# Kernel tuning notes

Measured on AMD Instinct MI355X. Metric: run time of the kernel, lower is better.

The kernel has to match this reference:

```python
import jax, jax.numpy as jnp
import numpy as np
from jax import lax

EPS = 1e-5

def _conv(x, w, stride, padding):
    # x: NCHW, w: OIHW
    return lax.conv_general_dilated(
        x, w, window_strides=(stride, stride), padding=padding,
        dimension_numbers=("NCHW", "OIHW", "NCHW"))

def _bn(x, gamma, beta):
    # BatchNorm2d in training mode: batch statistics over (N, H, W)
    mean = jnp.mean(x, axis=(0, 2, 3), keepdims=True)
    var = jnp.var(x, axis=(0, 2, 3), keepdims=True)
    inv = lax.rsqrt(var + EPS)
    g = gamma.reshape(1, -1, 1, 1)
    b = beta.reshape(1, -1, 1, 1)
    return (x - mean) * inv * g + b

def setup_inputs() -> dict:
    key = jax.random.key(0)
    ks = jax.random.split(key, 5)
    B, Cin, H, W = 128, 64, 56, 56
    Cout = 128
    x = jax.random.normal(ks[0], (B, Cin, H, W), dtype=jnp.float32)
    w1 = jax.random.normal(ks[1], (Cout, Cin, 3, 3), dtype=jnp.float32) * 0.05
    w2 = jax.random.normal(ks[2], (Cout, Cout, 3, 3), dtype=jnp.float32) * 0.05
    wd = jax.random.normal(ks[3], (Cout, Cin, 1, 1), dtype=jnp.float32) * 0.05
    g1 = jnp.ones((Cout,), jnp.float32); b1 = jnp.zeros((Cout,), jnp.float32)
    g2 = jnp.ones((Cout,), jnp.float32); b2 = jnp.zeros((Cout,), jnp.float32)
    gd = jnp.ones((Cout,), jnp.float32); bd = jnp.zeros((Cout,), jnp.float32)
    return {"x": x, "w1": w1, "g1": g1, "b1": b1,
            "w2": w2, "g2": g2, "b2": b2,
            "wd": wd, "gd": gd, "bd": bd}

def reference(x, w1, g1, b1, w2, g2, b2, wd, gd, bd):
    stride = 2
    # conv1 (3x3, stride=2, 'same') -> BN -> ReLU
    out = _conv(x, w1, stride, "SAME")
    out = jax.nn.relu(_bn(out, g1, b1))
    # conv2 (3x3, stride=1, 'same') -> BN
    out = _conv(out, w2, 1, "SAME")
    out = _bn(out, g2, b2)
    # downsample identity: 1x1 conv stride=2 'valid' -> BN
    identity = _bn(_conv(x, wd, stride, "VALID"), gd, bd)
    return jax.nn.relu(out + identity)
```

## Files before the change

### kernel.cpp

```cpp
#include <hip/hip_runtime.h>

constexpr int B = 128, Cin = 64, H = 56, W = 56;
constexpr int Cout = 128, Ho = 28, Wo = 28;
constexpr int HW = Ho * Wo;
constexpr int NPIX = B * HW;
constexpr int NOUT = NPIX * Cout;
constexpr int NBLK = NPIX / 128;
constexpr int NBLK2 = NPIX / 256;
constexpr float EPS_ = 1e-5f;
constexpr float CNT_ = (float)NPIX;

constexpr int HPX = 57, WPX = 57;
constexpr int HP1 = 30, WP1 = 30;

typedef __attribute__((ext_vector_type(8))) unsigned short u16x8;
typedef __attribute__((ext_vector_type(4))) unsigned short u16x4;
typedef __attribute__((ext_vector_type(8))) short bf16x8;
typedef __attribute__((ext_vector_type(4))) float f32x4;

__device__ inline float bf2f(unsigned short u) {
    union { unsigned int i; float f; } v; v.i = ((unsigned int)u) << 16; return v.f;
}
__device__ inline unsigned short f2bf(float f) {
    union { float f; unsigned int i; } v; v.f = f;
    return (unsigned short)((v.i + 0x7fffu + ((v.i >> 16) & 1u)) >> 16);
}

__device__ inline void gload16(const void* g, void* l) {
    __builtin_amdgcn_global_load_lds(
        (const __attribute__((address_space(1))) unsigned int*)g,
        (__attribute__((address_space(3))) unsigned int*)l, 16, 0, 0);
}

__global__ __launch_bounds__(512) void k_conv2_mfma(
        const unsigned short* __restrict__ xin,
        const unsigned short* __restrict__ wt,
        unsigned short* __restrict__ yout,
        float* __restrict__ part) {
    constexpr int CIN = 128, WP = 30, KTOT = 1152, NSTEP = 36;
    __shared__ unsigned short Alds[3][256 * 32];
    __shared__ unsigned short Blds[3][128 * 32];
    __shared__ float lsum[8][64], lsq[8][64];
    const int tid = threadIdx.x, w = tid >> 6, l = tid & 63;
    const int wr = w >> 1, wc = w & 1;
    const int bid = (blockIdx.x & 7) * (NBLK2 / 8) + (blockIdx.x >> 3);
    const int p0 = bid * 256;
    const char* xb = (const char*)xin;
    const char* wb = (const char*)wt;

    const int sslot = ((l & 3) ^ ((l >> 3) & 3)) * 16;
    const int rswz  = ((l >> 4) ^ ((l >> 1) & 3)) * 16;

    int gA[2], lofsA[2];
    #pragma unroll
    for (int i = 0; i < 2; ++i) {
        int row = w * 32 + i * 16 + (l >> 2);
        int p = p0 + row;
        int n = p / HW, rr = p % HW;
        int oh = rr / Wo, ow = rr % Wo;
        gA[i] = (((n * HP1 + oh) * WP + ow) * CIN) * 2 + sslot;
        lofsA[i] = row * 64 + (l & 3) * 16;
    }
    const int rowb = w * 16 + (l >> 2);
    const int gB = rowb * KTOT * 2 + sslot;
    const int lofsB = rowb * 64 + (l & 3) * 16;

    f32x4 acc[4][4];
    #pragma unroll
    for (int m = 0; m < 4; ++m)
        #pragma unroll
        for (int n = 0; n < 4; ++n)
            acc[m][n] = (f32x4){0.f, 0.f, 0.f, 0.f};

    gload16(xb + gA[0],      (char*)Alds[0] + lofsA[0]);
    gload16(xb + gA[1],      (char*)Alds[0] + lofsA[1]);
    gload16(wb + gB,         (char*)Blds[0] + lofsB);
    gload16(xb + gA[0] + 64, (char*)Alds[1] + lofsA[0]);
    gload16(xb + gA[1] + 64, (char*)Alds[1] + lofsA[1]);
    gload16(wb + gB + 64,    (char*)Blds[1] + lofsB);

    for (int oi = 0; oi < 3; ++oi) {
        const int Abase = oi * WP * CIN * 2;
        #pragma unroll
        for (int u = 0; u < 12; ++u) {
            const int s = oi * 12 + u;
            const int cur = u % 3;
            if (s + 1 < NSTEP) asm volatile("s_waitcnt vmcnt(3)" ::: "memory");
            else               asm volatile("s_waitcnt vmcnt(0)" ::: "memory");
            __builtin_amdgcn_s_barrier();
            if (s + 2 < NSTEP) {
                const int u2 = u + 2;
                const int j2 = u2 >> 2;
                const int c2 = u2 & 3;
                const int koffA = Abase + (j2 == 3 ? WP * CIN * 2 : j2 * CIN * 2) + c2 * 64;
                const int koffB = (s + 2) * 64;
                const int buf = u2 % 3;
                gload16(xb + gA[0] + koffA, (char*)Alds[buf] + lofsA[0]);
                gload16(xb + gA[1] + koffA, (char*)Alds[buf] + lofsA[1]);
                gload16(wb + gB + koffB,    (char*)Blds[buf] + lofsB);
            }
            bf16x8 bf[4];
            #pragma unroll
            for (int n = 0; n < 4; ++n)
                bf[n] = *(const bf16x8*)((const char*)Blds[cur] + (wc * 64 + n * 16 + (l & 15)) * 64 + rswz);
            #pragma unroll
            for (int m = 0; m < 4; ++m) {
                bf16x8 af = *(const bf16x8*)((const char*)Alds[cur] + (wr * 64 + m * 16 + (l & 15)) * 64 + rswz);
                #pragma unroll
                for (int n = 0; n < 4; ++n)
                    acc[m][n] = __builtin_amdgcn_mfma_f32_16x16x32_bf16(af, bf[n], acc[m][n], 0, 0, 0);
            }
        }
    }

    #pragma unroll
    for (int m = 0; m < 4; ++m) {
        int pq = p0 + wr * 64 + m * 16 + (l >> 4) * 4;
        int n = pq / HW, rr = pq % HW;
        #pragma unroll
        for (int q = 0; q < 4; ++q) {
            int co = wc * 64 + q * 16 + (l & 15);
            u16x4 v;
            #pragma unroll
            for (int r = 0; r < 4; ++r) v[r] = f2bf(acc[m][q][r]);
            *(u16x4*)(yout + ((size_t)(n * Cout + co)) * HW + rr) = v;
        }
    }

    float ps[4], pq_[4];
    #pragma unroll
    for (int n = 0; n < 4; ++n) {
        float s_ = 0.f, q_ = 0.f;
        #pragma unroll
        for (int m = 0; m < 4; ++m)
            #pragma unroll
            for (int r = 0; r < 4; ++r) { float v = acc[m][n][r]; s_ += v; q_ += v * v; }
        s_ += __shfl_xor(s_, 16); q_ += __shfl_xor(q_, 16);
        s_ += __shfl_xor(s_, 32); q_ += __shfl_xor(q_, 32);
        ps[n] = s_; pq_[n] = q_;
    }
    __syncthreads();
    if (l < 16) {
        #pragma unroll
        for (int n = 0; n < 4; ++n) { lsum[w][n * 16 + l] = ps[n]; lsq[w][n * 16 + l] = pq_[n]; }
    }
    __syncthreads();
    if (tid < 128) {
        int c = tid, half = c >> 6, j = c & 63;
        float s_ = 0.f, q_ = 0.f;
        #pragma unroll
        for (int r = 0; r < 4; ++r) { s_ += lsum[r * 2 + half][j]; q_ += lsq[r * 2 + half][j]; }
        part[((size_t)bid * 128 + c) * 2]     = s_;
        part[((size_t)bid * 128 + c) * 2 + 1] = q_;
    }
}

template<int STRIDE, int HP, int WP, int CIN, int KHW, bool OUTPAD, bool FUSE_DW>
__global__ __launch_bounds__(256) void k_conv_mfma(
        const unsigned short* __restrict__ xin,
        const unsigned short* __restrict__ wt,
        unsigned short* __restrict__ yout,
        float* __restrict__ part,
        const unsigned short* __restrict__ wtd,
        unsigned short* __restrict__ ydout,
        float* __restrict__ partd) {
    constexpr int KTOT = KHW * KHW * CIN;
    constexpr int NSTEP = KTOT / 32;
    constexpr int CSTEPS = CIN / 32;
    constexpr int RING = FUSE_DW ? 2 : 3;
    __shared__ unsigned short Alds[RING][128 * 32];
    __shared__ unsigned short Blds[RING][128 * 32];
    __shared__ unsigned short BdLds[FUSE_DW ? 2 * 128 * 32 : 4];
    __shared__ float lsum[4][64], lsq[4][64];
    const int tid = threadIdx.x, w = tid >> 6, l = tid & 63;
    const int wr = w >> 1, wc = w & 1;
    const int bid = (blockIdx.x & 7) * (NBLK / 8) + (blockIdx.x >> 3);
    const int p0 = bid * 128;
    const char* xb = (const char*)xin;
    const char* wb = (const char*)wt;
    const char* wdb = (const char*)wtd;

    const int sslot = ((l & 3) ^ ((l >> 3) & 3)) * 16;
    int gA[2], gB[2], gBd[2], lofs[2];
    #pragma unroll
    for (int i = 0; i < 2; ++i) {
        int row = w * 32 + i * 16 + (l >> 2);
        int p = p0 + row;
        int n = p / HW, rr = p % HW;
        int oh = rr / Wo, ow = rr % Wo;
        gA[i] = (((n * HP + oh * STRIDE) * WP + ow * STRIDE) * CIN) * 2 + sslot;
        gB[i] = (row * KTOT) * 2 + sslot;
        gBd[i] = row * 128 + sslot;
        lofs[i] = row * 64 + (l & 3) * 16;
    }

    f32x4 acc[4][4], accd[4][4];
    #pragma unroll
    for (int m = 0; m < 4; ++m)
        #pragma unroll
        for (int n = 0; n < 4; ++n) {
            acc[m][n] = (f32x4){0.f, 0.f, 0.f, 0.f};
            if constexpr (FUSE_DW) accd[m][n] = (f32x4){0.f, 0.f, 0.f, 0.f};
        }

    auto STAGE = [&](int s, int buf) {
        const int seg = s / CSTEPS;
        const int c0 = (s % CSTEPS) * 32;
        const int kh = seg / KHW, kw = seg % KHW;
        const int koffA = (((kh * WP + kw) * CIN) + c0) * 2;
        const int koffB = s * 64;
        gload16(xb + gA[0] + koffA, (char*)Alds[buf] + lofs[0]);
        gload16(xb + gA[1] + koffA, (char*)Alds[buf] + lofs[1]);
        gload16(wb + gB[0] + koffB, (char*)Blds[buf] + lofs[0]);
        gload16(wb + gB[1] + koffB, (char*)Blds[buf] + lofs[1]);
    };

    const int rswz = ((l >> 4) ^ ((l >> 1) & 3)) * 16;

    if constexpr (FUSE_DW) {
        #pragma unroll
        for (int s = 0; s < 2; ++s)
            #pragma unroll
            for (int i = 0; i < 2; ++i)
                gload16(wdb + gBd[i] + s * 64, (char*)BdLds + s * 8192 + lofs[i]);
    }
    STAGE(0, 0);
    if constexpr (!FUSE_DW) STAGE(1, 1);

    for (int s = 0; s < NSTEP; ++s) {
        const int cur = s % RING;
        if constexpr (FUSE_DW) {
            if (s + 1 < NSTEP) {
                STAGE(s + 1, (s + 1) % RING);
                asm volatile("s_waitcnt vmcnt(4)" ::: "memory");
            } else {
                asm volatile("s_waitcnt vmcnt(0)" ::: "memory");
            }
        } else {
            if (s + 2 < NSTEP) {
                STAGE(s + 2, (s + 2) % RING);
                asm volatile("s_waitcnt vmcnt(8)" ::: "memory");
            } else if (s + 1 < NSTEP) {
                asm volatile("s_waitcnt vmcnt(4)" ::: "memory");
            } else {
                asm volatile("s_waitcnt vmcnt(0)" ::: "memory");
            }
        }
        __builtin_amdgcn_s_barrier();
        bf16x8 af[4], bf[4];
        #pragma unroll
        for (int m = 0; m < 4; ++m)
            af[m] = *(const bf16x8*)((const char*)Alds[cur] + (wr * 64 + m * 16 + (l & 15)) * 64 + rswz);
        #pragma unroll
        for (int n = 0; n < 4; ++n)
            bf[n] = *(const bf16x8*)((const char*)Blds[cur] + (wc * 64 + n * 16 + (l & 15)) * 64 + rswz);
        #pragma unroll
        for (int m = 0; m < 4; ++m)
            #pragma unroll
            for (int n = 0; n < 4; ++n)
                acc[m][n] = __builtin_amdgcn_mfma_f32_16x16x32_bf16(af[m], bf[n], acc[m][n], 0, 0, 0);
        if constexpr (FUSE_DW) {
            if (s < CSTEPS) {
                bf16x8 bd[4];
                #pragma unroll
                for (int n = 0; n < 4; ++n)
                    bd[n] = *(const bf16x8*)((const char*)BdLds + s * 8192 + (wc * 64 + n * 16 + (l & 15)) * 64 + rswz);
                #pragma unroll
                for (int m = 0; m < 4; ++m)
                    #pragma unroll
                    for (int n = 0; n < 4; ++n)
                        accd[m][n] = __builtin_amdgcn_mfma_f32_16x16x32_bf16(af[m], bd[n], accd[m][n], 0, 0, 0);
            }
        }
        __builtin_amdgcn_s_barrier();
    }

    auto store_nchw = [&](f32x4 (&a)[4][4], unsigned short* yo) {
        #pragma unroll
        for (int m = 0; m < 4; ++m) {
            int pq = p0 + wr * 64 + m * 16 + (l >> 4) * 4;
            int n = pq / HW, rr = pq % HW;
            #pragma unroll
            for (int q = 0; q < 4; ++q) {
                int co = wc * 64 + q * 16 + (l & 15);
                u16x4 v;
                #pragma unroll
                for (int r = 0; r < 4; ++r) v[r] = f2bf(a[m][q][r]);
                *(u16x4*)(yo + ((size_t)(n * Cout + co)) * HW + rr) = v;
            }
        }
    };
    auto do_part = [&](f32x4 (&a)[4][4], float* pt) {
        float ps[4], pq_[4];
        #pragma unroll
        for (int n = 0; n < 4; ++n) {
            float s_ = 0.f, q_ = 0.f;
            #pragma unroll
            for (int m = 0; m < 4; ++m)
                #pragma unroll
                for (int r = 0; r < 4; ++r) { float v = a[m][n][r]; s_ += v; q_ += v * v; }
            s_ += __shfl_xor(s_, 16); q_ += __shfl_xor(q_, 16);
            s_ += __shfl_xor(s_, 32); q_ += __shfl_xor(q_, 32);
            ps[n] = s_; pq_[n] = q_;
        }
        __syncthreads();
        if (l < 16) {
            #pragma unroll
            for (int n = 0; n < 4; ++n) { lsum[w][n * 16 + l] = ps[n]; lsq[w][n * 16 + l] = pq_[n]; }
        }
        __syncthreads();
        if (tid < 128) {
            int c = tid, half = c >> 6, j = c & 63;
            pt[((size_t)bid * 128 + c) * 2]     = lsum[half][j] + lsum[half + 2][j];
            pt[((size_t)bid * 128 + c) * 2 + 1] = lsq[half][j] + lsq[half + 2][j];
        }
    };

    if constexpr (OUTPAD) {
        #pragma unroll
        for (int m = 0; m < 4; ++m) {
            #pragma unroll
            for (int r = 0; r < 4; ++r) {
                int p = p0 + wr * 64 + m * 16 + (l >> 4) * 4 + r;
                int n = p / HW, rr = p % HW;
                int oh = rr / Wo, ow = rr % Wo;
                unsigned short* dst = yout + ((size_t)((n * HP1 + oh + 1) * WP1 + ow + 1)) * 128
                                     + wc * 64 + (l & 15);
                #pragma unroll
                for (int q = 0; q < 4; ++q)
                    dst[q * 16] = f2bf(acc[m][q][r]);
            }
        }
    } else {
        store_nchw(acc, yout);
    }
    do_part(acc, part);
    if constexpr (FUSE_DW) {
        store_nchw(accd, ydout);
        do_part(accd, partd);
    }
}

__global__ __launch_bounds__(256) void k_zerob(unsigned short* __restrict__ xb,
                                               unsigned short* __restrict__ y1p) {
    int idx = blockIdx.x * 256 + threadIdx.x;
    constexpr int NA = B * 113 * 8;
    const u16x8 z = (u16x8){0, 0, 0, 0, 0, 0, 0, 0};
    if (idx < NA) {
        int cg = idx & 7; int t = idx >> 3;
        int bp = t % 113, n = t / 113;
        int ih = bp < 57 ? 56 : bp - 57;
        int iw = bp < 57 ? bp : 56;
        *(u16x8*)(xb + ((size_t)((n * HPX + ih) * WPX + iw)) * Cin + cg * 8) = z;
    } else {
        idx -= NA;
        if (idx >= B * 116 * 16) return;
        int cg = idx & 15; int t = idx >> 4;
        int bp = t % 116, n = t / 116;
        int oh, ow;
        if (bp < 30)      { oh = 0;           ow = bp; }
        else if (bp < 60) { oh = 29;          ow = bp - 30; }
        else if (bp < 88) { oh = bp - 60 + 1; ow = 0; }
        else              { oh = bp - 88 + 1; ow = 29; }
        *(u16x8*)(y1p + ((size_t)((n * HP1 + oh) * WP1 + ow)) * 128 + cg * 8) = z;
    }
}

__global__ __launch_bounds__(256) void k_xprep(const float* __restrict__ x,
                                               unsigned short* __restrict__ xb) {
    __shared__ unsigned short lds[64 * 57];
    int n = blockIdx.x / H, ih = blockIdx.x % H;
    const float* src = x + ((size_t)n * Cin * H + ih) * W;
    for (int j = threadIdx.x; j < Cin * W; j += 256) {
        int c = j / W, iw = j % W;
        lds[c * 57 + iw] = f2bf(src[(size_t)c * H * W + iw]);
    }
    __syncthreads();
    unsigned short* dst = xb + ((size_t)(n * HPX + ih)) * WPX * Cin;
    for (int k = threadIdx.x; k < W * 8; k += 256) {
        int pix = k >> 3, cg = k & 7;
        u16x8 v;
        #pragma unroll
        for (int e = 0; e < 8; ++e) v[e] = lds[(cg * 8 + e) * 57 + pix];
        *(u16x8*)(dst + pix * Cin + cg * 8) = v;
    }
}

__global__ void k_wprep_all(const float* __restrict__ w1, const float* __restrict__ w2,
                            const float* __restrict__ wd,
                            unsigned short* __restrict__ wt1, unsigned short* __restrict__ wt2,
                            unsigned short* __restrict__ wtd) {
    int idx = blockIdx.x * 256 + threadIdx.x;
    const float* w; unsigned short* wt; int cin, ntap;
    if (idx < 73728)            { w = w1; wt = wt1; cin = 64;  ntap = 9; }
    else if (idx < 73728 + 147456) { idx -= 73728; w = w2; wt = wt2; cin = 128; ntap = 9; }
    else if (idx < 73728 + 147456 + 8192) { idx -= 73728 + 147456; w = wd; wt = wtd; cin = 64; ntap = 1; }
    else return;
    int co = idx / (cin * ntap), r = idx % (cin * ntap);
    int ci = r / ntap, tap = r % ntap;
    wt[co * cin * ntap + tap * cin + ci] = f2bf(w[idx]);
}

__device__ inline void block_reduce2(float& s, float& s2) {
    #pragma unroll
    for (int off = 32; off > 0; off >>= 1) {
        s += __shfl_down(s, off);
        s2 += __shfl_down(s2, off);
    }
    __shared__ float ls[4], ls2[4];
    int wid = threadIdx.x >> 6, lane = threadIdx.x & 63;
    if (lane == 0) { ls[wid] = s; ls2[wid] = s2; }
    __syncthreads();
    if (threadIdx.x == 0) { s = ls[0] + ls[1] + ls[2] + ls[3]; s2 = ls2[0] + ls2[1] + ls2[2] + ls2[3]; }
}

__global__ __launch_bounds__(256) void k_finalize(
        const float* __restrict__ pA, const float* __restrict__ pB, int nA, int nB,
        const float* __restrict__ gA_, const float* __restrict__ bA_,
        const float* __restrict__ gB_, const float* __restrict__ bB_,
        float* __restrict__ scA, float* __restrict__ shA,
        float* __restrict__ scB, float* __restrict__ shB) {
    const bool second = blockIdx.x >= 128;
    const int c = blockIdx.x & 127;
    const float* part = second ? pB : pA;
    const int nblk = second ? nB : nA;
    const float* g = second ? gB_ : gA_;
    const float* b = second ? bB_ : bA_;
    float* scale = second ? scB : scA;
    float* shift = second ? shB : shA;
    float s = 0.f, q = 0.f;
    for (int k = threadIdx.x; k < nblk; k += 256) {
        s += part[((size_t)k * 128 + c) * 2];
        q += part[((size_t)k * 128 + c) * 2 + 1];
    }
    block_reduce2(s, q);
    if (threadIdx.x == 0) {
        float mean = s / CNT_;
        float var = q / CNT_ - mean * mean;
        float inv = rsqrtf(var + EPS_);
        scale[c] = g[c] * inv;
        shift[c] = b[c] - mean * g[c] * inv;
    }
}

__global__ __launch_bounds__(256) void k_bnrelu(unsigned short* __restrict__ y,
        const float* __restrict__ sc, const float* __restrict__ sh) {
    int t = threadIdx.x, cg = t & 15, pl = t >> 4;
    int p = blockIdx.x * 16 + pl;
    int n = p / HW, rr = p % HW;
    int oh = rr / Wo, ow = rr % Wo;
    size_t a = ((size_t)((n * HP1 + oh + 1) * WP1 + ow + 1)) * 128 + cg * 8;
    u16x8 v = *(u16x8*)(y + a);
    u16x8 o;
    #pragma unroll
    for (int e = 0; e < 8; ++e) {
        float f = bf2f(v[e]) * sc[cg * 8 + e] + sh[cg * 8 + e];
        o[e] = f2bf(fmaxf(f, 0.f));
    }
    *(u16x8*)(y + a) = o;
}

__global__ __launch_bounds__(256) void k_final(
        const unsigned short* __restrict__ y2, const unsigned short* __restrict__ yd,
        const float* __restrict__ sc2, const float* __restrict__ sh2,
        const float* __restrict__ scd, const float* __restrict__ shd,
        float* __restrict__ out) {
    int idx = blockIdx.x * 256 + threadIdx.x;
    int plane = idx / (HW / 8);
    int c = plane & (Cout - 1);
    int i = idx % (HW / 8);
    size_t a = (size_t)plane * HW + i * 8;
    u16x8 v2 = *(const u16x8*)(y2 + a);
    u16x8 vd = *(const u16x8*)(yd + a);
    float s2c = sc2[c], h2c = sh2[c], sdc = scd[c], hdc = shd[c];
    float4 r0, r1;
    r0.x = fmaxf(bf2f(v2[0]) * s2c + h2c + bf2f(vd[0]) * sdc + hdc, 0.f);
    r0.y = fmaxf(bf2f(v2[1]) * s2c + h2c + bf2f(vd[1]) * sdc + hdc, 0.f);
    r0.z = fmaxf(bf2f(v2[2]) * s2c + h2c + bf2f(vd[2]) * sdc + hdc, 0.f);
    r0.w = fmaxf(bf2f(v2[3]) * s2c + h2c + bf2f(vd[3]) * sdc + hdc, 0.f);
    r1.x = fmaxf(bf2f(v2[4]) * s2c + h2c + bf2f(vd[4]) * sdc + hdc, 0.f);
    r1.y = fmaxf(bf2f(v2[5]) * s2c + h2c + bf2f(vd[5]) * sdc + hdc, 0.f);
    r1.z = fmaxf(bf2f(v2[6]) * s2c + h2c + bf2f(vd[6]) * sdc + hdc, 0.f);
    r1.w = fmaxf(bf2f(v2[7]) * s2c + h2c + bf2f(vd[7]) * sdc + hdc, 0.f);
    *(float4*)(out + a) = r0;
    *(float4*)(out + a + 4) = r1;
}

extern "C" void kernel_launch(void* const* d_in, const int* in_sizes, int n_in,
                              void* d_out, int out_size, void* d_ws, size_t ws_size,
                              hipStream_t stream) {
    const float* x  = (const float*)d_in[0];
    const float* w1 = (const float*)d_in[1];
    const float* g1 = (const float*)d_in[2];
    const float* b1 = (const float*)d_in[3];
    const float* w2 = (const float*)d_in[4];
    const float* g2 = (const float*)d_in[5];
    const float* b2 = (const float*)d_in[6];
    const float* wd = (const float*)d_in[7];
    const float* gd = (const float*)d_in[8];
    const float* bd = (const float*)d_in[9];
    float* out = (float*)d_out;

    char* ws = (char*)d_ws;
    auto alloc = [&](size_t bytes) { char* p = ws; ws += (bytes + 255) & ~(size_t)255; return p; };
    unsigned short* xb  = (unsigned short*)alloc((size_t)B * HPX * WPX * Cin * 2);
    unsigned short* y1p = (unsigned short*)alloc((size_t)B * HP1 * WP1 * Cout * 2);
    unsigned short* y2b = (unsigned short*)alloc((size_t)NOUT * 2);
    unsigned short* ydb = (unsigned short*)alloc((size_t)NOUT * 2);
    unsigned short* wt1 = (unsigned short*)alloc((size_t)Cout * 576 * 2);
    unsigned short* wt2 = (unsigned short*)alloc((size_t)Cout * 1152 * 2);
    unsigned short* wtd = (unsigned short*)alloc((size_t)Cout * 64 * 2);
    float* part1 = (float*)alloc((size_t)NBLK * 128 * 2 * 4);
    float* part2 = (float*)alloc((size_t)NBLK2 * 128 * 2 * 4);
    float* partd = (float*)alloc((size_t)NBLK * 128 * 2 * 4);
    float* sc1 = (float*)alloc(128 * 4); float* sh1 = (float*)alloc(128 * 4);
    float* sc2 = (float*)alloc(128 * 4); float* sh2 = (float*)alloc(128 * 4);
    float* scd = (float*)alloc(128 * 4); float* shd = (float*)alloc(128 * 4);

    k_zerob<<<(B * 113 * 8 + B * 116 * 16 + 255) / 256, 256, 0, stream>>>(xb, y1p);
    k_xprep<<<B * H, 256, 0, stream>>>(x, xb);
    k_wprep_all<<<(73728 + 147456 + 8192 + 255) / 256, 256, 0, stream>>>(w1, w2, wd, wt1, wt2, wtd);

    k_conv_mfma<2, HPX, WPX, 64, 3, true, true><<<NBLK, 256, 0, stream>>>(
        xb, wt1, y1p, part1, wtd, ydb, partd);

    k_finalize<<<128, 256, 0, stream>>>(part1, part1, NBLK, NBLK,
                                        g1, b1, g1, b1, sc1, sh1, sc1, sh1);
    k_bnrelu<<<NPIX / 16, 256, 0, stream>>>(y1p, sc1, sh1);

    k_conv2_mfma<<<NBLK2, 512, 0, stream>>>(y1p, wt2, y2b, part2);

    k_finalize<<<256, 256, 0, stream>>>(part2, partd, NBLK2, NBLK,
                                        g2, b2, gd, bd, sc2, sh2, scd, shd);

    k_final<<<NOUT / 8 / 256, 256, 0, stream>>>(y2b, ydb, sc2, sh2, scd, shd, out);
}
```

Before: 175.4 us.

## Enlarge conv1 tile to 256 pixels with 512 threads and register-held downsample weights

The templated conv kernel becomes a dedicated conv1 kernel. It now uses 512-thread blocks covering 256 output pixels, so each block loads the weight tile once for twice as many pixels. The pipeline moves to a 3-deep ring with one barrier per step, and the 1x1 downsample weights stay in registers instead of LDS. The xprep kernel also handles two input rows per block with float4 loads. Together these aim to cut weight traffic, barrier overhead and launch count, at the cost of higher register and LDS pressure and fewer blocks.

```diff
diff --git a/kernel.cpp b/kernel.cpp
--- a/kernel.cpp
+++ b/kernel.cpp
@@ -5,7 +5,6 @@
 constexpr int HW = Ho * Wo;
 constexpr int NPIX = B * HW;
 constexpr int NOUT = NPIX * Cout;
-constexpr int NBLK = NPIX / 128;
 constexpr int NBLK2 = NPIX / 256;
 constexpr float EPS_ = 1e-5f;
 constexpr float CNT_ = (float)NPIX;
@@ -155,142 +154,132 @@
     }
 }
 
-template<int STRIDE, int HP, int WP, int CIN, int KHW, bool OUTPAD, bool FUSE_DW>
-__global__ __launch_bounds__(256) void k_conv_mfma(
+__global__ __launch_bounds__(512) void k_conv1_mfma(
         const unsigned short* __restrict__ xin,
         const unsigned short* __restrict__ wt,
+        const unsigned short* __restrict__ wtd,
         unsigned short* __restrict__ yout,
-        float* __restrict__ part,
-        const unsigned short* __restrict__ wtd,
         unsigned short* __restrict__ ydout,
-        float* __restrict__ partd) {
-    constexpr int KTOT = KHW * KHW * CIN;
-    constexpr int NSTEP = KTOT / 32;
-    constexpr int CSTEPS = CIN / 32;
-    constexpr int RING = FUSE_DW ? 2 : 3;
-    __shared__ unsigned short Alds[RING][128 * 32];
-    __shared__ unsigned short Blds[RING][128 * 32];
-    __shared__ unsigned short BdLds[FUSE_DW ? 2 * 128 * 32 : 4];
-    __shared__ float lsum[4][64], lsq[4][64];
+        float* __restrict__ part, float* __restrict__ partd) {
+    constexpr int CIN = 64, WP = 57, KTOT = 576, NSTEP = 18;
+    __shared__ unsigned short Alds[3][256 * 32];
+    __shared__ unsigned short Blds[3][128 * 32];
+    __shared__ float lsum[8][64], lsq[8][64];
     const int tid = threadIdx.x, w = tid >> 6, l = tid & 63;
     const int wr = w >> 1, wc = w & 1;
-    const int bid = (blockIdx.x & 7) * (NBLK / 8) + (blockIdx.x >> 3);
-    const int p0 = bid * 128;
+    const int bid = (blockIdx.x & 7) * (NBLK2 / 8) + (blockIdx.x >> 3);
+    const int p0 = bid * 256;
     const char* xb = (const char*)xin;
     const char* wb = (const char*)wt;
-    const char* wdb = (const char*)wtd;
 
     const int sslot = ((l & 3) ^ ((l >> 3) & 3)) * 16;
-    int gA[2], gB[2], gBd[2], lofs[2];
+    const int rswz  = ((l >> 4) ^ ((l >> 1) & 3)) * 16;
+
+    int gA[2], lofsA[2];
     #pragma unroll
     for (int i = 0; i < 2; ++i) {
         int row = w * 32 + i * 16 + (l >> 2);
         int p = p0 + row;
         int n = p / HW, rr = p % HW;
         int oh = rr / Wo, ow = rr % Wo;
-        gA[i] = (((n * HP + oh * STRIDE) * WP + ow * STRIDE) * CIN) * 2 + sslot;
-        gB[i] = (row * KTOT) * 2 + sslot;
-        gBd[i] = row * 128 + sslot;
-        lofs[i] = row * 64 + (l & 3) * 16;
-    }
+        gA[i] = (((n * HPX + oh * 2) * WP + ow * 2) * CIN) * 2 + sslot;
+        lofsA[i] = row * 64 + (l & 3) * 16;
+    }
+    const int rowb = w * 16 + (l >> 2);
+    const int gB = rowb * KTOT * 2 + sslot;
+    const int lofsB = rowb * 64 + (l & 3) * 16;
+
+    bf16x8 bd[2][4];
+    #pragma unroll
+    for (int s = 0; s < 2; ++s)
+        #pragma unroll
+        for (int n = 0; n < 4; ++n) {
+            int co = wc * 64 + n * 16 + (l & 15);
+            bd[s][n] = *(const bf16x8*)(wtd + co * 64 + s * 32 + (l >> 4) * 8);
+        }
 
     f32x4 acc[4][4], accd[4][4];
     #pragma unroll
     for (int m = 0; m < 4; ++m)
         #pragma unroll
         for (int n = 0; n < 4; ++n) {
-            acc[m][n] = (f32x4){0.f, 0.f, 0.f, 0.f};
-            if constexpr (FUSE_DW) accd[m][n] = (f32x4){0.f, 0.f, 0.f, 0.f};
-        }
-
-    auto STAGE = [&](int s, int buf) {
-        const int seg = s / CSTEPS;
-        const int c0 = (s % CSTEPS) * 32;
-        const int kh = seg / KHW, kw = seg % KHW;
-        const int koffA = (((kh * WP + kw) * CIN) + c0) * 2;
-        const int koffB = s * 64;
-        gload16(xb + gA[0] + koffA, (char*)Alds[buf] + lofs[0]);
-        gload16(xb + gA[1] + koffA, (char*)Alds[buf] + lofs[1]);
-        gload16(wb + gB[0] + koffB, (char*)Blds[buf] + lofs[0]);
-        gload16(wb + gB[1] + koffB, (char*)Blds[buf] + lofs[1]);
-    };
-
-    const int rswz = ((l >> 4) ^ ((l >> 1) & 3)) * 16;
-
-    if constexpr (FUSE_DW) {
-        #pragma unroll
-        for (int s = 0; s < 2; ++s)
-            #pragma unroll
-            for (int i = 0; i < 2; ++i)
-                gload16(wdb + gBd[i] + s * 64, (char*)BdLds + s * 8192 + lofs[i]);
-    }
-    STAGE(0, 0);
-    if constexpr (!FUSE_DW) STAGE(1, 1);
-
+            acc[m][n]  = (f32x4){0.f, 0.f, 0.f, 0.f};
+            accd[m][n] = (f32x4){0.f, 0.f, 0.f, 0.f};
+        }
+
+    #pragma unroll
+    for (int s = 0; s < 2; ++s) {
+        gload16(xb + gA[0] + s * 64, (char*)Alds[s] + lofsA[0]);
+        gload16(xb + gA[1] + s * 64, (char*)Alds[s] + lofsA[1]);
+        gload16(wb + gB + s * 64,    (char*)Blds[s] + lofsB);
+    }
+
+    #pragma unroll
     for (int s = 0; s < NSTEP; ++s) {
-        const int cur = s % RING;
-        if constexpr (FUSE_DW) {
-            if (s + 1 < NSTEP) {
-                STAGE(s + 1, (s + 1) % RING);
-                asm volatile("s_waitcnt vmcnt(4)" ::: "memory");
-            } else {
-                asm volatile("s_waitcnt vmcnt(0)" ::: "memory");
-            }
-        } else {
-            if (s + 2 < NSTEP) {
-                STAGE(s + 2, (s + 2) % RING);
-                asm volatile("s_waitcnt vmcnt(8)" ::: "memory");
-            } else if (s + 1 < NSTEP) {
-                asm volatile("s_waitcnt vmcnt(4)" ::: "memory");
-            } else {
-                asm volatile("s_waitcnt vmcnt(0)" ::: "memory");
-            }
-        }
+        const int cur = s % 3;
+        if (s + 1 < NSTEP) asm volatile("s_waitcnt vmcnt(3)" ::: "memory");
+        else               asm volatile("s_waitcnt vmcnt(0)" ::: "memory");
         __builtin_amdgcn_s_barrier();
-        bf16x8 af[4], bf[4];
-        #pragma unroll
-        for (int m = 0; m < 4; ++m)
-            af[m] = *(const bf16x8*)((const char*)Alds[cur] + (wr * 64 + m * 16 + (l & 15)) * 64 + rswz);
+        if (s + 2 < NSTEP) {
+            const int s2 = s + 2;
+            const int seg = s2 >> 1, kh = seg / 3, kw = seg % 3;
+            const int koffA = (kh * WP + kw) * CIN * 2 + (s2 & 1) * 64;
+            const int koffB = s2 * 64;
+            const int buf = s2 % 3;
+            gload16(xb + gA[0] + koffA, (char*)Alds[buf] + lofsA[0]);
+            gload16(xb + gA[1] + koffA, (char*)Alds[buf] + lofsA[1]);
+            gload16(wb + gB + koffB,    (char*)Blds[buf] + lofsB);
+        }
+        bf16x8 bf[4];
         #pragma unroll
         for (int n = 0; n < 4; ++n)
             bf[n] = *(const bf16x8*)((const char*)Blds[cur] + (wc * 64 + n * 16 + (l & 15)) * 64 + rswz);
         #pragma unroll
-        for (int m = 0; m < 4; ++m)
+        for (int m = 0; m < 4; ++m) {
+            bf16x8 af = *(const bf16x8*)((const char*)Alds[cur] + (wr * 64 + m * 16 + (l & 15)) * 64 + rswz);
             #pragma unroll
             for (int n = 0; n < 4; ++n)
-                acc[m][n] = __builtin_amdgcn_mfma_f32_16x16x32_bf16(af[m], bf[n], acc[m][n], 0, 0, 0);
-        if constexpr (FUSE_DW) {
-            if (s < CSTEPS) {
-                bf16x8 bd[4];
+                acc[m][n] = __builtin_amdgcn_mfma_f32_16x16x32_bf16(af, bf[n], acc[m][n], 0, 0, 0);
+            if (s < 2) {
                 #pragma unroll
                 for (int n = 0; n < 4; ++n)
-                    bd[n] = *(const bf16x8*)((const char*)BdLds + s * 8192 + (wc * 64 + n * 16 + (l & 15)) * 64 + rswz);
-                #pragma unroll
-                for (int m = 0; m < 4; ++m)
-                    #pragma unroll
-                    for (int n = 0; n < 4; ++n)
-                        accd[m][n] = __builtin_amdgcn_mfma_f32_16x16x32_bf16(af[m], bd[n], accd[m][n], 0, 0, 0);
+                    accd[m][n] = __builtin_amdgcn_mfma_f32_16x16x32_bf16(af, bd[s][n], accd[m][n], 0, 0, 0);
             }
         }
-        __builtin_amdgcn_s_barrier();
-    }
-
-    auto store_nchw = [&](f32x4 (&a)[4][4], unsigned short* yo) {
-        #pragma unroll
-        for (int m = 0; m < 4; ++m) {
-            int pq = p0 + wr * 64 + m * 16 + (l >> 4) * 4;
-            int n = pq / HW, rr = pq % HW;
-            #pragma unroll
-            for (int q = 0; q < 4; ++q) {
-                int co = wc * 64 + q * 16 + (l & 15);
-                u16x4 v;
-                #pragma unroll
-                for (int r = 0; r < 4; ++r) v[r] = f2bf(a[m][q][r]);
-                *(u16x4*)(yo + ((size_t)(n * Cout + co)) * HW + rr) = v;
-            }
-        }
-    };
-    auto do_part = [&](f32x4 (&a)[4][4], float* pt) {
+    }
+
+    #pragma unroll
+    for (int m = 0; m < 4; ++m) {
+        #pragma unroll
+        for (int r = 0; r < 4; ++r) {
+            int p = p0 + wr * 64 + m * 16 + (l >> 4) * 4 + r;
+            int n = p / HW, rr = p % HW;
+            int oh = rr / Wo, ow = rr % Wo;
+            unsigned short* dst = yout + ((size_t)((n * HP1 + oh + 1) * WP1 + ow + 1)) * 128
+                                 + wc * 64 + (l & 15);
+            #pragma unroll
+            for (int q = 0; q < 4; ++q)
+                dst[q * 16] = f2bf(acc[m][q][r]);
+        }
+    }
+    #pragma unroll
+    for (int m = 0; m < 4; ++m) {
+        int pq = p0 + wr * 64 + m * 16 + (l >> 4) * 4;
+        int n = pq / HW, rr = pq % HW;
+        #pragma unroll
+        for (int q = 0; q < 4; ++q) {
+            int co = wc * 64 + q * 16 + (l & 15);
+            u16x4 v;
+            #pragma unroll
+            for (int r = 0; r < 4; ++r) v[r] = f2bf(accd[m][q][r]);
+            *(u16x4*)(ydout + ((size_t)(n * Cout + co)) * HW + rr) = v;
+        }
+    }
+
+    #pragma unroll
+    for (int pass = 0; pass < 2; ++pass) {
+        f32x4 (&a)[4][4] = pass ? accd : acc;
+        float* pt = pass ? partd : part;
         float ps[4], pq_[4];
         #pragma unroll
         for (int n = 0; n < 4; ++n) {
@@ -311,33 +300,12 @@
         __syncthreads();
         if (tid < 128) {
             int c = tid, half = c >> 6, j = c & 63;
-            pt[((size_t)bid * 128 + c) * 2]     = lsum[half][j] + lsum[half + 2][j];
-            pt[((size_t)bid * 128 + c) * 2 + 1] = lsq[half][j] + lsq[half + 2][j];
-        }
-    };
-
-    if constexpr (OUTPAD) {
-        #pragma unroll
-        for (int m = 0; m < 4; ++m) {
-            #pragma unroll
-            for (int r = 0; r < 4; ++r) {
-                int p = p0 + wr * 64 + m * 16 + (l >> 4) * 4 + r;
-                int n = p / HW, rr = p % HW;
-                int oh = rr / Wo, ow = rr % Wo;
-                unsigned short* dst = yout + ((size_t)((n * HP1 + oh + 1) * WP1 + ow + 1)) * 128
-                                     + wc * 64 + (l & 15);
-                #pragma unroll
-                for (int q = 0; q < 4; ++q)
-                    dst[q * 16] = f2bf(acc[m][q][r]);
-            }
-        }
-    } else {
-        store_nchw(acc, yout);
-    }
-    do_part(acc, part);
-    if constexpr (FUSE_DW) {
-        store_nchw(accd, ydout);
-        do_part(accd, partd);
+            float s_ = 0.f, q_ = 0.f;
+            #pragma unroll
+            for (int r = 0; r < 4; ++r) { s_ += lsum[r * 2 + half][j]; q_ += lsq[r * 2 + half][j]; }
+            pt[((size_t)bid * 128 + c) * 2]     = s_;
+            pt[((size_t)bid * 128 + c) * 2 + 1] = q_;
+        }
     }
 }
 
@@ -366,23 +334,26 @@
     }
 }
 
-__global__ __launch_bounds__(256) void k_xprep(const float* __restrict__ x,
+__global__ __launch_bounds__(512) void k_xprep(const float* __restrict__ x,
                                                unsigned short* __restrict__ xb) {
-    __shared__ unsigned short lds[64 * 57];
-    int n = blockIdx.x / H, ih = blockIdx.x % H;
-    const float* src = x + ((size_t)n * Cin * H + ih) * W;
-    for (int j = threadIdx.x; j < Cin * W; j += 256) {
-        int c = j / W, iw = j % W;
-        lds[c * 57 + iw] = f2bf(src[(size_t)c * H * W + iw]);
+    __shared__ unsigned short lds[2][64 * 57];
+    int n = blockIdx.x / (H / 2), ihp = blockIdx.x % (H / 2), ih0 = ihp * 2;
+    const float* src = x + ((size_t)n * Cin * H + ih0) * W;
+    for (int j = threadIdx.x; j < 2 * Cin * 14; j += 512) {
+        int r = j / 896, rem = j % 896;
+        int c = rem / 14, q = rem % 14;
+        float4 v = *(const float4*)(src + ((size_t)c * H + r) * W + q * 4);
+        unsigned short* d = &lds[r][c * 57 + q * 4];
+        d[0] = f2bf(v.x); d[1] = f2bf(v.y); d[2] = f2bf(v.z); d[3] = f2bf(v.w);
     }
     __syncthreads();
-    unsigned short* dst = xb + ((size_t)(n * HPX + ih)) * WPX * Cin;
-    for (int k = threadIdx.x; k < W * 8; k += 256) {
-        int pix = k >> 3, cg = k & 7;
+    for (int k = threadIdx.x; k < 2 * W * 8; k += 512) {
+        int r = k / 448, k2 = k % 448;
+        int pix = k2 >> 3, cg = k2 & 7;
         u16x8 v;
         #pragma unroll
-        for (int e = 0; e < 8; ++e) v[e] = lds[(cg * 8 + e) * 57 + pix];
-        *(u16x8*)(dst + pix * Cin + cg * 8) = v;
+        for (int e = 0; e < 8; ++e) v[e] = lds[r][(cg * 8 + e) * 57 + pix];
+        *(u16x8*)(xb + ((size_t)((n * HPX + ih0 + r) * WPX + pix)) * Cin + cg * 8) = v;
     }
 }
 
@@ -510,27 +481,26 @@
     unsigned short* wt1 = (unsigned short*)alloc((size_t)Cout * 576 * 2);
     unsigned short* wt2 = (unsigned short*)alloc((size_t)Cout * 1152 * 2);
     unsigned short* wtd = (unsigned short*)alloc((size_t)Cout * 64 * 2);
-    float* part1 = (float*)alloc((size_t)NBLK * 128 * 2 * 4);
+    float* part1 = (float*)alloc((size_t)NBLK2 * 128 * 2 * 4);
     float* part2 = (float*)alloc((size_t)NBLK2 * 128 * 2 * 4);
-    float* partd = (float*)alloc((size_t)NBLK * 128 * 2 * 4);
+    float* partd = (float*)alloc((size_t)NBLK2 * 128 * 2 * 4);
     float* sc1 = (float*)alloc(128 * 4); float* sh1 = (float*)alloc(128 * 4);
     float* sc2 = (float*)alloc(128 * 4); float* sh2 = (float*)alloc(128 * 4);
     float* scd = (float*)alloc(128 * 4); float* shd = (float*)alloc(128 * 4);
 
     k_zerob<<<(B * 113 * 8 + B * 116 * 16 + 255) / 256, 256, 0, stream>>>(xb, y1p);
-    k_xprep<<<B * H, 256, 0, stream>>>(x, xb);
+    k_xprep<<<B * (H / 2), 512, 0, stream>>>(x, xb);
     k_wprep_all<<<(73728 + 147456 + 8192 + 255) / 256, 256, 0, stream>>>(w1, w2, wd, wt1, wt2, wtd);
 
-    k_conv_mfma<2, HPX, WPX, 64, 3, true, true><<<NBLK, 256, 0, stream>>>(
-        xb, wt1, y1p, part1, wtd, ydb, partd);
-
-    k_finalize<<<128, 256, 0, stream>>>(part1, part1, NBLK, NBLK,
+    k_conv1_mfma<<<NBLK2, 512, 0, stream>>>(xb, wt1, wtd, y1p, ydb, part1, partd);
+
+    k_finalize<<<128, 256, 0, stream>>>(part1, part1, NBLK2, NBLK2,
                                         g1, b1, g1, b1, sc1, sh1, sc1, sh1);
     k_bnrelu<<<NPIX / 16, 256, 0, stream>>>(y1p, sc1, sh1);
 
     k_conv2_mfma<<<NBLK2, 512, 0, stream>>>(y1p, wt2, y2b, part2);
 
-    k_finalize<<<256, 256, 0, stream>>>(part2, partd, NBLK2, NBLK,
+    k_finalize<<<256, 256, 0, stream>>>(part2, partd, NBLK2, NBLK2,
                                         g2, b2, gd, bd, sc2, sh2, scd, shd);
 
     k_final<<<NOUT / 8 / 256, 256, 0, stream>>>(y2b, ydb, sc2, sh2, scd, shd, out);
```

New measurement: 164.3 us (median of 3 runs). -6.3%, faster.
